# Kernel tuning notes

Measured on AMD Instinct MI355X. Metric: run time of the kernel, lower is better.

## Reference

```python
import jax, jax.numpy as jnp
import numpy as np

NUM_USERS = 1_000_000
NUM_ITEMS = 100_000
NUM_GROUPS = 500_000
EMB = 32           # forced by reshape (1, 4*32)
GROUP_SIZE = 3     # forced: 3 members + 1 item = 4 rows
B = 131_072


def setup_inputs() -> dict:
    key = jax.random.key(0)
    ks = jax.random.split(key, 12)
    return {
        "group_inputs": jax.random.randint(ks[0], (B,), 0, NUM_GROUPS),
        "item_inputs": jax.random.randint(ks[1], (B,), 0, NUM_ITEMS),
        "members": jax.random.randint(ks[2], (NUM_GROUPS, GROUP_SIZE), 0, NUM_USERS),
        "user_emb": jax.random.normal(ks[3], (NUM_USERS, EMB), jnp.float32) * 0.05,
        "item_emb": jax.random.normal(ks[4], (NUM_ITEMS, EMB - 18), jnp.float32) * 0.05,
        "genres": jax.random.uniform(ks[5], (NUM_ITEMS, 18), jnp.float32),
        "attn_W": jax.random.normal(ks[6], (4 * EMB, 3), jnp.float32) * 0.05,
        "attn_b": jax.random.normal(ks[7], (3,), jnp.float32) * 0.05,
        "pred_W1": jax.random.normal(ks[8], (3 * EMB, 8), jnp.float32) * 0.05,
        "pred_b1": jax.random.normal(ks[9], (8,), jnp.float32) * 0.05,
        "pred_W2": jax.random.normal(ks[10], (8, 1), jnp.float32) * 0.05,
        "pred_b2": jax.random.normal(ks[11], (1,), jnp.float32) * 0.05,
    }


def reference(group_inputs, item_inputs, members, user_emb, item_emb, genres,
              attn_W, attn_b, pred_W1, pred_b1, pred_W2, pred_b2):
    # item embedding: 14-d latent concat 18-d genre features -> [B, 32]
    it_e = jnp.concatenate([item_emb[item_inputs], genres[item_inputs]], axis=1)
    # members of each group -> [B, 3, 32]
    mem_e = user_emb[members[group_inputs]]
    # concat 3 member rows + 1 item row, flatten to [B, 128]
    gi = jnp.concatenate([mem_e, it_e[:, None, :]], axis=1).reshape(-1, 4 * EMB)
    # NOTE: source ConcatAttentionLayer returns the raw linear output (softmax
    # is computed but discarded), so attention "weights" are raw logits. [B, 3]
    at_wt = gi @ attn_W + attn_b
    # weighted sum of member embeddings -> [B, 32]
    g = jnp.einsum("bk,bkd->bd", at_wt, mem_e)
    new = jnp.concatenate([g * it_e, g, it_e], axis=1)  # [B, 96]
    h = jax.nn.relu(new @ pred_W1 + pred_b1)
    y = jax.nn.sigmoid(h @ pred_W2 + pred_b2)  # [B, 1]
    return y
```

## Files before the change

kernel.cpp:

```cpp
#include <hip/hip_runtime.h>
#include <math.h>

#define EMB 32

__global__ __launch_bounds__(256, 2) void bahdanau_fused(
    const int* __restrict__ group_inputs,
    const int* __restrict__ item_inputs,
    const int* __restrict__ members,
    const float* __restrict__ user_emb,
    const float* __restrict__ item_emb,
    const float* __restrict__ genres,
    const float* __restrict__ attn_W,
    const float* __restrict__ attn_b,
    const float* __restrict__ pred_W1,
    const float* __restrict__ pred_b1,
    const float* __restrict__ pred_W2,
    const float* __restrict__ pred_b2,
    float* __restrict__ out)
{
    __shared__ float s_aW[128 * 3];
    __shared__ float s_W1[96 * 8];
    __shared__ float s_ab[3];
    __shared__ float s_b1[8];
    __shared__ float s_W2[8];
    __shared__ float s_b2[1];

    const int tid = threadIdx.x;
    for (int i = tid; i < 384; i += 256) s_aW[i] = attn_W[i];
    for (int i = tid; i < 768; i += 256) s_W1[i] = pred_W1[i];
    if (tid < 3) s_ab[tid] = attn_b[tid];
    if (tid >= 4 && tid < 12) s_b1[tid - 4] = pred_b1[tid - 4];
    if (tid >= 12 && tid < 20) s_W2[tid - 12] = pred_W2[tid - 12];
    if (tid == 20) s_b2[0] = pred_b2[0];
    __syncthreads();

    const int t = tid & 3;
    const int grp = tid >> 2;
    const int ebase = blockIdx.x * 256 + grp * 4;
    const int dbase = t * 8;

    const int emine = ebase + t;
    const int gidx = group_inputs[emine];
    const int iidx = item_inputs[emine];
    const int mm0 = members[3 * gidx + 0];
    const int mm1 = members[3 * gidx + 1];
    const int mm2 = members[3 * gidx + 2];

    int itq[4], mq[4][3];
#pragma unroll
    for (int q = 0; q < 4; ++q) {
        itq[q]   = __shfl(iidx, q, 4);
        mq[q][0] = __shfl(mm0, q, 4);
        mq[q][1] = __shfl(mm1, q, 4);
        mq[q][2] = __shfl(mm2, q, 4);
    }

    float mem[4][3][8];
#pragma unroll
    for (int q = 0; q < 4; ++q)
#pragma unroll
        for (int j = 0; j < 3; ++j) {
            const float4* p =
                (const float4*)(user_emb + (size_t)mq[q][j] * EMB + dbase);
            float4 lo = p[0];
            float4 hi = p[1];
            mem[q][j][0] = lo.x; mem[q][j][1] = lo.y;
            mem[q][j][2] = lo.z; mem[q][j][3] = lo.w;
            mem[q][j][4] = hi.x; mem[q][j][5] = hi.y;
            mem[q][j][6] = hi.z; mem[q][j][7] = hi.w;
        }

    float itv[4][8];
#pragma unroll
    for (int q = 0; q < 4; ++q)
#pragma unroll
        for (int i = 0; i < 8; ++i) {
            int d = dbase + i;
            const float* p = (d < 14)
                ? (item_emb + (size_t)itq[q] * 14 + d)
                : (genres + (size_t)itq[q] * 18 + (d - 14));
            itv[q][i] = *p;
        }

    float aw[4][3];
#pragma unroll
    for (int q = 0; q < 4; ++q) { aw[q][0] = 0.f; aw[q][1] = 0.f; aw[q][2] = 0.f; }

#pragma unroll
    for (int i = 0; i < 8; ++i) {
        float w[4][3];
#pragma unroll
        for (int j = 0; j < 4; ++j) {
            int row = j * 32 + dbase + i;
            w[j][0] = s_aW[row * 3 + 0];
            w[j][1] = s_aW[row * 3 + 1];
            w[j][2] = s_aW[row * 3 + 2];
        }
#pragma unroll
        for (int q = 0; q < 4; ++q)
#pragma unroll
            for (int k = 0; k < 3; ++k)
                aw[q][k] += mem[q][0][i] * w[0][k] + mem[q][1][i] * w[1][k]
                          + mem[q][2][i] * w[2][k] + itv[q][i] * w[3][k];
    }
#pragma unroll
    for (int q = 0; q < 4; ++q)
#pragma unroll
        for (int k = 0; k < 3; ++k) {
            float v = aw[q][k];
            v += __shfl_xor(v, 1, 4);
            v += __shfl_xor(v, 2, 4);
            aw[q][k] = v + s_ab[k];
        }

    float gv[4][8];
#pragma unroll
    for (int q = 0; q < 4; ++q)
#pragma unroll
        for (int i = 0; i < 8; ++i)
            gv[q][i] = aw[q][0] * mem[q][0][i] + aw[q][1] * mem[q][1][i]
                     + aw[q][2] * mem[q][2][i];

    float ph[4][8];
#pragma unroll
    for (int q = 0; q < 4; ++q)
#pragma unroll
        for (int c = 0; c < 8; ++c) ph[q][c] = 0.f;

#pragma unroll
    for (int i = 0; i < 8; ++i) {
        int d = dbase + i;
        float w0[8], w1[8], w2[8];
#pragma unroll
        for (int c = 0; c < 8; ++c) {
            w0[c] = s_W1[d * 8 + c];
            w1[c] = s_W1[(32 + d) * 8 + c];
            w2[c] = s_W1[(64 + d) * 8 + c];
        }
#pragma unroll
        for (int q = 0; q < 4; ++q) {
            float a = gv[q][i] * itv[q][i];
            float b = gv[q][i];
            float cc = itv[q][i];
#pragma unroll
            for (int c = 0; c < 8; ++c)
                ph[q][c] += a * w0[c] + b * w1[c] + cc * w2[c];
        }
    }

    float hq[8];
#pragma unroll
    for (int q = 0; q < 4; ++q)
#pragma unroll
        for (int c = 0; c < 8; ++c) {
            float v = ph[q][c];
            v += __shfl_xor(v, 1, 4);
            v += __shfl_xor(v, 2, 4);
            if (q == t) hq[c] = v;
        }

    float y = s_b2[0];
#pragma unroll
    for (int c = 0; c < 8; ++c) {
        float h = hq[c] + s_b1[c];
        h = fmaxf(h, 0.0f);
        y = fmaf(h, s_W2[c], y);
    }
    y = 1.0f / (1.0f + expf(-y));
    out[ebase + t] = y;
}

extern "C" void kernel_launch(void* const* d_in, const int* in_sizes, int n_in,
                              void* d_out, int out_size, void* d_ws, size_t ws_size,
                              hipStream_t stream) {
    const int*   group_inputs = (const int*)d_in[0];
    const int*   item_inputs  = (const int*)d_in[1];
    const int*   members      = (const int*)d_in[2];
    const float* user_emb     = (const float*)d_in[3];
    const float* item_emb     = (const float*)d_in[4];
    const float* genres       = (const float*)d_in[5];
    const float* attn_W       = (const float*)d_in[6];
    const float* attn_b       = (const float*)d_in[7];
    const float* pred_W1      = (const float*)d_in[8];
    const float* pred_b1      = (const float*)d_in[9];
    const float* pred_W2      = (const float*)d_in[10];
    const float* pred_b2      = (const float*)d_in[11];
    float* out = (float*)d_out;

    const int B = in_sizes[0];
    const int blocks = B / 256;

    bahdanau_fused<<<blocks, 256, 0, stream>>>(
        group_inputs, item_inputs, members, user_emb, item_emb, genres,
        attn_W, attn_b, pred_W1, pred_b1, pred_W2, pred_b2, out);
}
```

Measured before the change: 215.0 us.

## Halve per-thread work to two rows, transpose weights in LDS, raise occupancy

Result: no change. 214.9 us (-0.0%).

```diff
diff --git a/kernel.cpp b/kernel.cpp
--- a/kernel.cpp
+++ b/kernel.cpp
@@ -3,7 +3,7 @@
 
 #define EMB 32
 
-__global__ __launch_bounds__(256, 2) void bahdanau_fused(
+__global__ __launch_bounds__(256, 4) void bahdanau_fused(
     const int* __restrict__ group_inputs,
     const int* __restrict__ item_inputs,
     const int* __restrict__ members,
@@ -18,156 +18,161 @@
     const float* __restrict__ pred_b2,
     float* __restrict__ out)
 {
-    __shared__ float s_aW[128 * 3];
-    __shared__ float s_W1[96 * 8];
+    __shared__ float s_aWT[3 * 128];
+    __shared__ float s_W1T[8 * 96];
     __shared__ float s_ab[3];
     __shared__ float s_b1[8];
     __shared__ float s_W2[8];
     __shared__ float s_b2[1];
 
     const int tid = threadIdx.x;
-    for (int i = tid; i < 384; i += 256) s_aW[i] = attn_W[i];
-    for (int i = tid; i < 768; i += 256) s_W1[i] = pred_W1[i];
+    for (int i = tid; i < 3 * 128; i += 256) {
+        int k = i >> 7, d = i & 127;
+        s_aWT[i] = attn_W[d * 3 + k];
+    }
+    for (int i = tid; i < 8 * 96; i += 256) {
+        int c = i / 96, r = i - c * 96;
+        s_W1T[i] = pred_W1[r * 8 + c];
+    }
     if (tid < 3) s_ab[tid] = attn_b[tid];
-    if (tid >= 4 && tid < 12) s_b1[tid - 4] = pred_b1[tid - 4];
-    if (tid >= 12 && tid < 20) s_W2[tid - 12] = pred_W2[tid - 12];
-    if (tid == 20) s_b2[0] = pred_b2[0];
+    else if (tid < 11) s_b1[tid - 3] = pred_b1[tid - 3];
+    else if (tid < 19) s_W2[tid - 11] = pred_W2[tid - 11];
+    else if (tid == 19) s_b2[0] = pred_b2[0];
     __syncthreads();
 
     const int t = tid & 3;
     const int grp = tid >> 2;
-    const int ebase = blockIdx.x * 256 + grp * 4;
+    const int ebase = blockIdx.x * 128 + grp * 2;
     const int dbase = t * 8;
 
-    const int emine = ebase + t;
-    const int gidx = group_inputs[emine];
-    const int iidx = item_inputs[emine];
-    const int mm0 = members[3 * gidx + 0];
-    const int mm1 = members[3 * gidx + 1];
-    const int mm2 = members[3 * gidx + 2];
-
-    int itq[4], mq[4][3];
-#pragma unroll
-    for (int q = 0; q < 4; ++q) {
-        itq[q]   = __shfl(iidx, q, 4);
-        mq[q][0] = __shfl(mm0, q, 4);
-        mq[q][1] = __shfl(mm1, q, 4);
-        mq[q][2] = __shfl(mm2, q, 4);
-    }
-
-    float mem[4][3][8];
-#pragma unroll
-    for (int q = 0; q < 4; ++q)
-#pragma unroll
-        for (int j = 0; j < 3; ++j) {
-            const float4* p =
-                (const float4*)(user_emb + (size_t)mq[q][j] * EMB + dbase);
-            float4 lo = p[0];
-            float4 hi = p[1];
-            mem[q][j][0] = lo.x; mem[q][j][1] = lo.y;
-            mem[q][j][2] = lo.z; mem[q][j][3] = lo.w;
-            mem[q][j][4] = hi.x; mem[q][j][5] = hi.y;
-            mem[q][j][6] = hi.z; mem[q][j][7] = hi.w;
-        }
-
-    float itv[4][8];
-#pragma unroll
-    for (int q = 0; q < 4; ++q)
-#pragma unroll
-        for (int i = 0; i < 8; ++i) {
-            int d = dbase + i;
-            const float* p = (d < 14)
-                ? (item_emb + (size_t)itq[q] * 14 + d)
-                : (genres + (size_t)itq[q] * 18 + (d - 14));
-            itv[q][i] = *p;
-        }
-
-    float aw[4][3];
-#pragma unroll
-    for (int q = 0; q < 4; ++q) { aw[q][0] = 0.f; aw[q][1] = 0.f; aw[q][2] = 0.f; }
-
-#pragma unroll
-    for (int i = 0; i < 8; ++i) {
-        float w[4][3];
-#pragma unroll
-        for (int j = 0; j < 4; ++j) {
-            int row = j * 32 + dbase + i;
-            w[j][0] = s_aW[row * 3 + 0];
-            w[j][1] = s_aW[row * 3 + 1];
-            w[j][2] = s_aW[row * 3 + 2];
-        }
-#pragma unroll
-        for (int q = 0; q < 4; ++q)
-#pragma unroll
-            for (int k = 0; k < 3; ++k)
-                aw[q][k] += mem[q][0][i] * w[0][k] + mem[q][1][i] * w[1][k]
-                          + mem[q][2][i] * w[2][k] + itv[q][i] * w[3][k];
-    }
-#pragma unroll
-    for (int q = 0; q < 4; ++q)
-#pragma unroll
-        for (int k = 0; k < 3; ++k) {
-            float v = aw[q][k];
-            v += __shfl_xor(v, 1, 4);
-            v += __shfl_xor(v, 2, 4);
-            aw[q][k] = v + s_ab[k];
-        }
-
-    float gv[4][8];
-#pragma unroll
-    for (int q = 0; q < 4; ++q)
-#pragma unroll
-        for (int i = 0; i < 8; ++i)
-            gv[q][i] = aw[q][0] * mem[q][0][i] + aw[q][1] * mem[q][1][i]
-                     + aw[q][2] * mem[q][2][i];
-
-    float ph[4][8];
-#pragma unroll
-    for (int q = 0; q < 4; ++q)
-#pragma unroll
-        for (int c = 0; c < 8; ++c) ph[q][c] = 0.f;
-
+    const int g0 = group_inputs[ebase], g1 = group_inputs[ebase + 1];
+    const int i0 = item_inputs[ebase],  i1 = item_inputs[ebase + 1];
+    int m0[3], m1[3];
+#pragma unroll
+    for (int j = 0; j < 3; ++j) {
+        m0[j] = members[3 * g0 + j];
+        m1[j] = members[3 * g1 + j];
+    }
+
+    float mem0[3][8], mem1[3][8];
+#pragma unroll
+    for (int j = 0; j < 3; ++j) {
+        const float4* p0 = (const float4*)(user_emb + (size_t)m0[j] * EMB + dbase);
+        const float4* p1 = (const float4*)(user_emb + (size_t)m1[j] * EMB + dbase);
+        float4 a = p0[0], b = p0[1], c = p1[0], d = p1[1];
+        mem0[j][0] = a.x; mem0[j][1] = a.y; mem0[j][2] = a.z; mem0[j][3] = a.w;
+        mem0[j][4] = b.x; mem0[j][5] = b.y; mem0[j][6] = b.z; mem0[j][7] = b.w;
+        mem1[j][0] = c.x; mem1[j][1] = c.y; mem1[j][2] = c.z; mem1[j][3] = c.w;
+        mem1[j][4] = d.x; mem1[j][5] = d.y; mem1[j][6] = d.z; mem1[j][7] = d.w;
+    }
+
+    float itv0[8], itv1[8];
 #pragma unroll
     for (int i = 0; i < 8; ++i) {
         int d = dbase + i;
-        float w0[8], w1[8], w2[8];
+        const float* p0 = (d < 14) ? item_emb + (size_t)i0 * 14 + d
+                                   : genres + (size_t)i0 * 18 + (d - 14);
+        const float* p1 = (d < 14) ? item_emb + (size_t)i1 * 14 + d
+                                   : genres + (size_t)i1 * 18 + (d - 14);
+        itv0[i] = *p0;
+        itv1[i] = *p1;
+    }
+
+    float aw0[3], aw1[3];
+#pragma unroll
+    for (int k = 0; k < 3; ++k) {
+        float a0 = 0.f, a1 = 0.f;
+#pragma unroll
+        for (int j = 0; j < 3; ++j) {
+            const float4* wp = (const float4*)&s_aWT[k * 128 + j * 32 + dbase];
+            float4 wl = wp[0], wh = wp[1];
+            float w[8] = {wl.x, wl.y, wl.z, wl.w, wh.x, wh.y, wh.z, wh.w};
+#pragma unroll
+            for (int i = 0; i < 8; ++i) {
+                a0 = fmaf(mem0[j][i], w[i], a0);
+                a1 = fmaf(mem1[j][i], w[i], a1);
+            }
+        }
+        {
+            const float4* wp = (const float4*)&s_aWT[k * 128 + 96 + dbase];
+            float4 wl = wp[0], wh = wp[1];
+            float w[8] = {wl.x, wl.y, wl.z, wl.w, wh.x, wh.y, wh.z, wh.w};
+#pragma unroll
+            for (int i = 0; i < 8; ++i) {
+                a0 = fmaf(itv0[i], w[i], a0);
+                a1 = fmaf(itv1[i], w[i], a1);
+            }
+        }
+        aw0[k] = a0; aw1[k] = a1;
+    }
+#pragma unroll
+    for (int k = 0; k < 3; ++k) {
+        float v0 = aw0[k];
+        v0 += __shfl_xor(v0, 1, 4);
+        v0 += __shfl_xor(v0, 2, 4);
+        aw0[k] = v0 + s_ab[k];
+        float v1 = aw1[k];
+        v1 += __shfl_xor(v1, 1, 4);
+        v1 += __shfl_xor(v1, 2, 4);
+        aw1[k] = v1 + s_ab[k];
+    }
+
+    float gv0[8], gv1[8], git0[8], git1[8];
+#pragma unroll
+    for (int i = 0; i < 8; ++i) {
+        gv0[i] = aw0[0] * mem0[0][i] + aw0[1] * mem0[1][i] + aw0[2] * mem0[2][i];
+        gv1[i] = aw1[0] * mem1[0][i] + aw1[1] * mem1[1][i] + aw1[2] * mem1[2][i];
+        git0[i] = gv0[i] * itv0[i];
+        git1[i] = gv1[i] * itv1[i];
+    }
+
+    float ph0[8], ph1[8];
+#pragma unroll
+    for (int c = 0; c < 8; ++c) {
+        float a0 = 0.f, a1 = 0.f;
+        const float4* wp0 = (const float4*)&s_W1T[c * 96 + dbase];
+        const float4* wp1 = (const float4*)&s_W1T[c * 96 + 32 + dbase];
+        const float4* wp2 = (const float4*)&s_W1T[c * 96 + 64 + dbase];
+        float4 al = wp0[0], ah = wp0[1];
+        float4 bl = wp1[0], bh = wp1[1];
+        float4 cl = wp2[0], ch = wp2[1];
+        float wa[8] = {al.x, al.y, al.z, al.w, ah.x, ah.y, ah.z, ah.w};
+        float wb[8] = {bl.x, bl.y, bl.z, bl.w, bh.x, bh.y, bh.z, bh.w};
+        float wc[8] = {cl.x, cl.y, cl.z, cl.w, ch.x, ch.y, ch.z, ch.w};
+#pragma unroll
+        for (int i = 0; i < 8; ++i) {
+            a0 = fmaf(git0[i], wa[i], a0);
+            a0 = fmaf(gv0[i],  wb[i], a0);
+            a0 = fmaf(itv0[i], wc[i], a0);
+            a1 = fmaf(git1[i], wa[i], a1);
+            a1 = fmaf(gv1[i],  wb[i], a1);
+            a1 = fmaf(itv1[i], wc[i], a1);
+        }
+        ph0[c] = a0; ph1[c] = a1;
+    }
+
+    float hq[8];
+#pragma unroll
+    for (int c = 0; c < 8; ++c) {
+        float v0 = ph0[c];
+        v0 += __shfl_xor(v0, 1, 4);
+        v0 += __shfl_xor(v0, 2, 4);
+        float v1 = ph1[c];
+        v1 += __shfl_xor(v1, 1, 4);
+        v1 += __shfl_xor(v1, 2, 4);
+        hq[c] = (t == 0) ? v0 : v1;
+    }
+
+    if (t < 2) {
+        float y = s_b2[0];
 #pragma unroll
         for (int c = 0; c < 8; ++c) {
-            w0[c] = s_W1[d * 8 + c];
-            w1[c] = s_W1[(32 + d) * 8 + c];
-            w2[c] = s_W1[(64 + d) * 8 + c];
-        }
-#pragma unroll
-        for (int q = 0; q < 4; ++q) {
-            float a = gv[q][i] * itv[q][i];
-            float b = gv[q][i];
-            float cc = itv[q][i];
-#pragma unroll
-            for (int c = 0; c < 8; ++c)
-                ph[q][c] += a * w0[c] + b * w1[c] + cc * w2[c];
-        }
-    }
-
-    float hq[8];
-#pragma unroll
-    for (int q = 0; q < 4; ++q)
-#pragma unroll
-        for (int c = 0; c < 8; ++c) {
-            float v = ph[q][c];
-            v += __shfl_xor(v, 1, 4);
-            v += __shfl_xor(v, 2, 4);
-            if (q == t) hq[c] = v;
-        }
-
-    float y = s_b2[0];
-#pragma unroll
-    for (int c = 0; c < 8; ++c) {
-        float h = hq[c] + s_b1[c];
-        h = fmaxf(h, 0.0f);
-        y = fmaf(h, s_W2[c], y);
-    }
-    y = 1.0f / (1.0f + expf(-y));
-    out[ebase + t] = y;
+            float h = fmaxf(hq[c] + s_b1[c], 0.0f);
+            y = fmaf(h, s_W2[c], y);
+        }
+        y = 1.0f / (1.0f + expf(-y));
+        out[ebase + t] = y;
+    }
 }
 
 extern "C" void kernel_launch(void* const* d_in, const int* in_sizes, int n_in,
@@ -188,7 +193,7 @@
     float* out = (float*)d_out;
 
     const int B = in_sizes[0];
-    const int blocks = B / 256;
+    const int blocks = B / 128;
 
     bahdanau_fused<<<blocks, 256, 0, stream>>>(
         group_inputs, item_inputs, members, user_emb, item_emb, genres,
```
